# Kernel optimization log

Hardware: AMD Instinct MI355X
Metric: run time of the kernel (lower is better)

## Reference

```python
import jax, jax.numpy as jnp
import numpy as np
from jax import lax

T, Nn, K, IN, H1, H2, G, P, HEADS = 64, 2048, 32, 256, 128, 128, 256, 60, 3


def setup_inputs() -> dict:
    key = jax.random.key(0)
    ks = jax.random.split(key, 20)
    s = 0.05  # weight scale to keep activations sane
    return {
        'h': jax.random.normal(ks[0], (T, Nn, IN), jnp.float32),
        'neigh': jax.random.randint(ks[1], (Nn, K), 0, Nn),
        'Npop': jnp.ones((1,), jnp.float32) * 1e6,
        'I': jax.random.uniform(ks[2], (T,), jnp.float32) * 1e4,
        'R': jax.random.uniform(ks[3], (T,), jnp.float32) * 1e4,
        'S': jax.random.uniform(ks[4], (T,), jnp.float32) * 9e5,
        'It': jax.random.uniform(ks[5], (T,), jnp.float32),
        'Rt': jax.random.uniform(ks[6], (T,), jnp.float32),
        'fc1': jax.random.normal(ks[7], (HEADS, IN, H1), jnp.float32) * s,
        'fc2': jax.random.normal(ks[8], (HEADS * H1, H2), jnp.float32) * s,
        'gru_Wih': jax.random.normal(ks[9], (3 * G, H2), jnp.float32) * s,
        'gru_Whh': jax.random.normal(ks[10], (3 * G, G), jnp.float32) * s,
        'gru_bih': jax.random.normal(ks[11], (3 * G,), jnp.float32) * s,
        'gru_bhh': jax.random.normal(ks[12], (3 * G,), jnp.float32) * s,
        'res1_W': jax.random.normal(ks[13], (2 * P, G + 2), jnp.float32) * s,
        'res1_b': jax.random.normal(ks[14], (2 * P,), jnp.float32) * s,
        'res2_W': jax.random.normal(ks[15], (2, G + 2), jnp.float32) * s,
        'res2_b': jax.random.normal(ks[16], (2,), jnp.float32) * s,
        'hx0': jax.random.normal(ks[17], (G,), jnp.float32),
    }


def _input_attention(iz, neigh):
    # cosine^4 edge scores, unnormalized weighted sum of neighbor feats
    src = iz[neigh]                                  # [N,K,d]
    dot = jnp.einsum('nkd,nd->nk', src, iz)
    nsrc = jnp.sqrt(jnp.einsum('nkd,nkd->nk', src, src))
    ndst = jnp.sqrt(jnp.sum(iz * iz, axis=-1))[:, None]
    e = (dot / nsrc / ndst) ** 4                     # [N,K]
    return jnp.einsum('nk,nkd->nd', e, src)


def _gat_head(x, W, neigh):
    # dot-product edge attention + per-node softmax + weighted reduce
    z = x @ W                                        # [N,H]
    src = z[neigh]                                   # [N,K,H]
    e = jnp.einsum('nkd,nd->nk', src, z)             # [N,K]
    a = jax.nn.softmax(e, axis=1)
    return jnp.einsum('nk,nkd->nd', a, src)


def _gru_cell(x, hx, Wih, Whh, bih, bhh):
    gi = Wih @ x + bih                               # [3G]
    gh = Whh @ hx + bhh
    ir, iz, inn = jnp.split(gi, 3)
    hr, hz, hn = jnp.split(gh, 3)
    r = jax.nn.sigmoid(ir + hr)
    zg = jax.nn.sigmoid(iz + hz)
    n = jnp.tanh(inn + r * hn)
    return (1.0 - zg) * n + zg * hx


def reference(h, neigh, Npop, I, R, S, It, Rt, fc1, fc2, gru_Wih, gru_Whh,
              gru_bih, gru_bhh, res1_W, res1_b, res2_W, res2_b, hx0):
    Np = Npop[0]

    def step(hx, xs):
        h_t, I_t, R_t, S_t, It_t, Rt_t = xs
        ih = _input_attention(h_t, neigh)                       # [N,in]
        heads = jax.vmap(lambda W: _gat_head(ih, W, neigh))(fc1)  # [3,N,H1]
        c = jax.nn.relu(jnp.transpose(heads, (1, 0, 2)).reshape(Nn, HEADS * H1))
        c = _gat_head(c, fc2, neigh)                            # [N,H2]
        pooled = jnp.max(jax.nn.relu(c), axis=0)                # [H2]
        hx = _gru_cell(pooled, hx, gru_Wih, gru_Whh, gru_bih, gru_bhh)
        nhx = jnp.concatenate([hx, It_t[None], Rt_t[None]])     # [G+2]
        pred = res1_W @ nhx + res1_b                            # [2P]
        ab = res2_W @ nhx + res2_b
        a_s = jax.nn.sigmoid(ab[0])
        b_s = jax.nn.sigmoid(ab[1])
        new_I = pred[0::2]
        new_R = pred[1::2]

        def sir(st, _):
            lI, lR, lS = st
            dI = a_s * lI * (lS / Np) - b_s * lI
            dR = b_s * lI
            nI = lI + lax.stop_gradient(dI)
            nR = lR + lax.stop_gradient(dR)
            nS = Np - nI - nR
            return (nI, nR, nS), (dI, dR)

        _, (pI, pR) = lax.scan(sir, (I_t, R_t, S_t), None, length=P)
        return hx, (new_I, new_R, pI, pR)

    _, (new_I, new_R, phy_I, phy_R) = lax.scan(step, hx0, (h, I, R, S, It, Rt))
    return (new_I, new_R, phy_I.reshape(-1), phy_R.reshape(-1))
```

## Files before the change

### kernel.cpp

```cpp
#include <hip/hip_runtime.h>
#include <hip/hip_bf16.h>
#include <math.h>

#define T_STEPS 64
#define NN      2048
#define KN      32
#define IND     256
#define H1D     128
#define C1D     384
#define H2D     128
#define GD      256
#define PD      60
#define GRU_NB  8

#define BITREV5_INIT {0,16,8,24,4,20,12,28,2,18,10,26,6,22,14,30, \
                      1,17,9,25,5,21,13,29,3,19,11,27,7,23,15,31}

__device__ __forceinline__ float xpose_reduce16(float part[16], int lane) {
#pragma unroll
    for (int i = 0; i < 8; ++i) {
        float send = (lane & 2) ? part[i] : part[i + 8];
        float keep = (lane & 2) ? part[i + 8] : part[i];
        part[i] = keep + __shfl_xor(send, 2);
    }
#pragma unroll
    for (int i = 0; i < 4; ++i) {
        float send = (lane & 4) ? part[i] : part[i + 4];
        float keep = (lane & 4) ? part[i + 4] : part[i];
        part[i] = keep + __shfl_xor(send, 4);
    }
#pragma unroll
    for (int i = 0; i < 2; ++i) {
        float send = (lane & 8) ? part[i] : part[i + 2];
        float keep = (lane & 8) ? part[i + 2] : part[i];
        part[i] = keep + __shfl_xor(send, 8);
    }
    {
        float send = (lane & 16) ? part[0] : part[1];
        float keep = (lane & 16) ? part[1] : part[0];
        part[0] = keep + __shfl_xor(send, 16);
    }
    return part[0] + __shfl_xor(part[0], 32);
}

__global__ __launch_bounds__(256) void norms_kernel(const float* __restrict__ h,
                                                    float* __restrict__ norms,
                                                    int t_base) {
    int gw   = (int)((blockIdx.x * blockDim.x + threadIdx.x) >> 6);
    int lane = threadIdx.x & 63;
    int n    = gw & (NN - 1);
    int tloc = gw >> 11;
    const float* row = h + ((size_t)(t_base + tloc) * NN + n) * IND;
    float s = 0.f;
#pragma unroll
    for (int q = 0; q < 4; ++q) { float v = row[lane + 64 * q]; s += v * v; }
#pragma unroll
    for (int off = 32; off > 0; off >>= 1) s += __shfl_xor(s, off);
    if (lane == 0) norms[(size_t)tloc * NN + n] = sqrtf(s);
}

__global__ __launch_bounds__(256) void input_attn_kernel(const float* __restrict__ h,
                                                         const int* __restrict__ neigh,
                                                         const float* __restrict__ norms,
                                                         float* __restrict__ ih,
                                                         int t_base) {
    const int BR[32] = BITREV5_INIT;
    __shared__ float hd_s[2][2][32];
    int wave    = threadIdx.x >> 6;
    int nodeloc = wave >> 1;
    int half    = wave & 1;
    int lane    = threadIdx.x & 63;
    int gw   = (int)((blockIdx.x << 1) | nodeloc);
    int n    = gw & (NN - 1);
    int tloc = gw >> 11;
    const float* hT  = h + (size_t)(t_base + tloc) * NN * IND;
    const float* nrm = norms + (size_t)tloc * NN;

    const float* dst = hT + (size_t)n * IND + half * 128;
    float d0 = dst[lane], d1 = dst[lane + 64];

    int   jreg = neigh[n * KN + (lane & 31)];
    float nj   = nrm[jreg];
    float ndst = nrm[n];

    float r0[32], r1[32], comb[16];
#pragma unroll
    for (int i = 0; i < 16; ++i) {
        int ja = __shfl(jreg, BR[i]);
        int jb = __shfl(jreg, BR[i + 16]);
        const float* sa = hT + (size_t)ja * IND + half * 128;
        const float* sb = hT + (size_t)jb * IND + half * 128;
        r0[i]      = sa[lane]; r1[i]      = sa[lane + 64];
        r0[i + 16] = sb[lane]; r1[i + 16] = sb[lane + 64];
        float pa = r0[i] * d0 + r1[i] * d1;
        float pb = r0[i + 16] * d0 + r1[i + 16] * d1;
        float send = (lane & 1) ? pa : pb;
        float keep = (lane & 1) ? pb : pa;
        comb[i] = keep + __shfl_xor(send, 1);
    }
    float hdot = xpose_reduce16(comb, lane);
    if (lane < 32) hd_s[nodeloc][half][lane] = hdot;
    __syncthreads();
    float dot = hdot + hd_s[nodeloc][half ^ 1][lane & 31];

    float r  = dot / (nj * ndst);
    float r2 = r * r;
    float e  = r2 * r2;

    float a0 = 0.f, a1 = 0.f;
#pragma unroll
    for (int i = 0; i < 32; ++i) {
        float ek = __shfl(e, BR[i]);
        a0 += ek * r0[i];
        a1 += ek * r1[i];
    }
    float* orow = ih + (size_t)gw * IND + half * 128;
    orow[lane]      = a0;
    orow[lane + 64] = a1;
}

__global__ __launch_bounds__(256) void matmul_f32(const float* __restrict__ A,
                                                  const float* __restrict__ B,
                                                  float* __restrict__ C,
                                                  int M, int N, int K) {
    __shared__ float As[16][65];
    __shared__ float Bs[16][68];
    int tid  = threadIdx.x;
    int row0 = blockIdx.y * 64;
    int col0 = blockIdx.x * 64;
    int tr = tid >> 4, tc = tid & 15;
    float acc[4][4] = {};
    int la_m = tid >> 2;
    int la_k = (tid & 3) * 4;
    int lb_k = tid >> 4;
    int lb_n = (tid & 15) * 4;
    for (int k0 = 0; k0 < K; k0 += 16) {
        float4 av = *(const float4*)(A + (size_t)(row0 + la_m) * K + k0 + la_k);
        float4 bv = *(const float4*)(B + (size_t)(k0 + lb_k) * N + col0 + lb_n);
        __syncthreads();
        As[la_k + 0][la_m] = av.x; As[la_k + 1][la_m] = av.y;
        As[la_k + 2][la_m] = av.z; As[la_k + 3][la_m] = av.w;
        *(float4*)&Bs[lb_k][lb_n] = bv;
        __syncthreads();
#pragma unroll
        for (int kk = 0; kk < 16; ++kk) {
            float a[4], b[4];
#pragma unroll
            for (int r = 0; r < 4; ++r) a[r] = As[kk][tr * 4 + r];
#pragma unroll
            for (int c = 0; c < 4; ++c) b[c] = Bs[kk][tc * 4 + c];
#pragma unroll
            for (int r = 0; r < 4; ++r)
#pragma unroll
                for (int c = 0; c < 4; ++c) acc[r][c] += a[r] * b[c];
        }
    }
#pragma unroll
    for (int r = 0; r < 4; ++r) {
        float4 v = { acc[r][0], acc[r][1], acc[r][2], acc[r][3] };
        *(float4*)(C + (size_t)(row0 + tr * 4 + r) * N + col0 + tc * 4) = v;
    }
}

__global__ __launch_bounds__(192) void gat_heads_kernel(const float* __restrict__ z1,
                                                        const int* __restrict__ neigh,
                                                        float* __restrict__ c) {
    const int BR[32] = BITREV5_INIT;
    int n    = blockIdx.x & (NN - 1);
    const float* ztbl = z1 + (size_t)(blockIdx.x >> 11) * NN * C1D;
    int head = threadIdx.x >> 6;
    int lane = threadIdx.x & 63;

    const float* dst = ztbl + (size_t)n * C1D + head * H1D;
    float d0 = dst[lane], d1 = dst[lane + 64];
    int jreg = neigh[n * KN + (lane & 31)];

    float r0[32], r1[32], comb[16];
#pragma unroll
    for (int i = 0; i < 16; ++i) {
        int ja = __shfl(jreg, BR[i]);
        int jb = __shfl(jreg, BR[i + 16]);
        const float* sa = ztbl + (size_t)ja * C1D + head * H1D;
        const float* sb = ztbl + (size_t)jb * C1D + head * H1D;
        r0[i]      = sa[lane]; r1[i]      = sa[lane + 64];
        r0[i + 16] = sb[lane]; r1[i + 16] = sb[lane + 64];
        float pa = r0[i] * d0 + r1[i] * d1;
        float pb = r0[i + 16] * d0 + r1[i + 16] * d1;
        float send = (lane & 1) ? pa : pb;
        float keep = (lane & 1) ? pb : pa;
        comb[i] = keep + __shfl_xor(send, 1);
    }
    float dot = xpose_reduce16(comb, lane);

    float m = dot;
#pragma unroll
    for (int off = 16; off > 0; off >>= 1) m = fmaxf(m, __shfl_xor(m, off));
    float p = __expf(dot - m);
    float s = p;
#pragma unroll
    for (int off = 16; off > 0; off >>= 1) s += __shfl_xor(s, off);
    p /= s;

    float a0 = 0.f, a1 = 0.f;
#pragma unroll
    for (int i = 0; i < 32; ++i) {
        float pk = __shfl(p, BR[i]);
        a0 += pk * r0[i];
        a1 += pk * r1[i];
    }
    size_t base = (size_t)blockIdx.x * C1D + (size_t)head * H1D;
    c[base + lane]      = fmaxf(a0, 0.f);
    c[base + lane + 64] = fmaxf(a1, 0.f);
}

__global__ __launch_bounds__(256) void gat_final_kernel(const float* __restrict__ z2,
                                                        const int* __restrict__ neigh,
                                                        float* __restrict__ c2) {
    const int BR[32] = BITREV5_INIT;
    int gw   = (int)((blockIdx.x << 2) | (threadIdx.x >> 6));
    int n    = gw & (NN - 1);
    const float* ztbl = z2 + (size_t)(gw >> 11) * NN * H2D;
    int lane = threadIdx.x & 63;

    const float* dst = ztbl + (size_t)n * H2D;
    float d0 = dst[lane], d1 = dst[lane + 64];
    int jreg = neigh[n * KN + (lane & 31)];

    float r0[32], r1[32], comb[16];
#pragma unroll
    for (int i = 0; i < 16; ++i) {
        int ja = __shfl(jreg, BR[i]);
        int jb = __shfl(jreg, BR[i + 16]);
        const float* sa = ztbl + (size_t)ja * H2D;
        const float* sb = ztbl + (size_t)jb * H2D;
        r0[i]      = sa[lane]; r1[i]      = sa[lane + 64];
        r0[i + 16] = sb[lane]; r1[i + 16] = sb[lane + 64];
        float pa = r0[i] * d0 + r1[i] * d1;
        float pb = r0[i + 16] * d0 + r1[i + 16] * d1;
        float send = (lane & 1) ? pa : pb;
        float keep = (lane & 1) ? pb : pa;
        comb[i] = keep + __shfl_xor(send, 1);
    }
    float dot = xpose_reduce16(comb, lane);

    float m = dot;
#pragma unroll
    for (int off = 16; off > 0; off >>= 1) m = fmaxf(m, __shfl_xor(m, off));
    float p = __expf(dot - m);
    float s = p;
#pragma unroll
    for (int off = 16; off > 0; off >>= 1) s += __shfl_xor(s, off);
    p /= s;

    float a0 = 0.f, a1 = 0.f;
#pragma unroll
    for (int i = 0; i < 32; ++i) {
        float pk = __shfl(p, BR[i]);
        a0 += pk * r0[i];
        a1 += pk * r1[i];
    }
    c2[(size_t)gw * H2D + lane]      = fmaxf(a0, 0.f);
    c2[(size_t)gw * H2D + lane + 64] = fmaxf(a1, 0.f);
}

__global__ __launch_bounds__(128) void pool_part_kernel(const float* __restrict__ c2,
                                                        float* __restrict__ ppart) {
    int j = threadIdx.x;
    int tloc  = blockIdx.x >> 4;
    int slice = blockIdx.x & 15;
    const float* base = c2 + ((size_t)tloc * NN + slice * 128) * H2D;
    float mx = 0.f;
    for (int q = 0; q < 128; ++q) mx = fmaxf(mx, base[(size_t)q * H2D + j]);
    ppart[(size_t)blockIdx.x * H2D + j] = mx;
}
__global__ __launch_bounds__(128) void pool_reduce_kernel(const float* __restrict__ ppart,
                                                          float* __restrict__ pooled,
                                                          int t_base) {
    int j = threadIdx.x;
    const float* base = ppart + (size_t)blockIdx.x * 16 * H2D;
    float mx = 0.f;
#pragma unroll
    for (int q = 0; q < 16; ++q) mx = fmaxf(mx, base[(size_t)q * H2D + j]);
    pooled[(t_base + blockIdx.x) * H2D + j] = mx;
}

__global__ void prep_W1(const float* __restrict__ fc1, float* __restrict__ W1,
                        unsigned int* __restrict__ cnt) {
    int i = blockIdx.x * 256 + threadIdx.x;
    if (i < 256 * 384) {
        int d = i / 384, cf = i % 384;
        int hd = cf >> 7, j = cf & 127;
        W1[i] = fc1[(size_t)hd * 256 * 128 + (size_t)d * 128 + j];
    }
    if (i < T_STEPS) cnt[i] = 0u;
}

__global__ __launch_bounds__(256) void gi_all_kernel(const float* __restrict__ Wih,
                                                     const float* __restrict__ bih,
                                                     const float* __restrict__ pooled,
                                                     float* __restrict__ gi_all) {
    __shared__ float p_s[H2D];
    int t  = blockIdx.x / 3;
    int ob = (blockIdx.x % 3) * 256;
    if (threadIdx.x < H2D) p_s[threadIdx.x] = pooled[t * H2D + threadIdx.x];
    __syncthreads();
    int o = ob + threadIdx.x;
    float acc = bih[o];
    const float* wr = Wih + (size_t)o * H2D;
#pragma unroll 4
    for (int d = 0; d < H2D; ++d) acc += wr[d] * p_s[d];
    gi_all[t * 768 + o] = acc;
}

__global__ __launch_bounds__(768) void gru_reg_kernel(const float* __restrict__ Whh,
                                                      const float* __restrict__ bhh,
                                                      const float* __restrict__ gi_all,
                                                      const float* __restrict__ hx0,
                                                      float* hx_all,
                                                      unsigned int* cnt) {
    __shared__ float4 hx_pad[72];
    __shared__ __align__(16) float hx_lin[GD];
    __shared__ float gh_s[96];
    int b   = blockIdx.x;
    int tid = threadIdx.x;
    int row_local = tid >> 3;
    int sub       = tid & 7;
    int chunk     = row_local >> 5;
    int r_in      = row_local & 31;
    int grow      = chunk * GD + b * 32 + r_in;

    float4 wreg[8];
    const float4* wrow = (const float4*)(Whh + (size_t)grow * GD + sub * 32);
#pragma unroll
    for (int i = 0; i < 8; ++i) wreg[i] = wrow[i];
    float bias = (sub == 0) ? bhh[grow] : 0.f;

    for (int t = 0; t < T_STEPS; ++t) {
        if (t > 0) {
            if (tid == 0) {
                while (__hip_atomic_load(&cnt[t - 1], __ATOMIC_ACQUIRE,
                                         __HIP_MEMORY_SCOPE_AGENT) < GRU_NB)
                    __builtin_amdgcn_s_sleep(1);
            }
            __syncthreads();
        }
        const float* hsrc = (t == 0) ? hx0 : (hx_all + (size_t)(t - 1) * GD);
        if (tid < 64) {
            float4 v;
            v.x = __hip_atomic_load(hsrc + tid * 4 + 0, __ATOMIC_RELAXED, __HIP_MEMORY_SCOPE_AGENT);
            v.y = __hip_atomic_load(hsrc + tid * 4 + 1, __ATOMIC_RELAXED, __HIP_MEMORY_SCOPE_AGENT);
            v.z = __hip_atomic_load(hsrc + tid * 4 + 2, __ATOMIC_RELAXED, __HIP_MEMORY_SCOPE_AGENT);
            v.w = __hip_atomic_load(hsrc + tid * 4 + 3, __ATOMIC_RELAXED, __HIP_MEMORY_SCOPE_AGENT);
            hx_pad[(tid >> 3) * 9 + (tid & 7)] = v;
            ((float4*)hx_lin)[tid] = v;
        }
        __syncthreads();

        float acc = 0.f;
#pragma unroll
        for (int i = 0; i < 8; ++i) {
            float4 hv = hx_pad[sub * 9 + i];
            float4 wv = wreg[i];
            acc += wv.x * hv.x + wv.y * hv.y + wv.z * hv.z + wv.w * hv.w;
        }
        acc += __shfl_xor(acc, 1);
        acc += __shfl_xor(acc, 2);
        acc += __shfl_xor(acc, 4);
        if (sub == 0) gh_s[row_local] = acc + bias;
        __syncthreads();

        if (tid < 32) {
            int u = b * 32 + tid;
            float gi_r = gi_all[t * 768 + u];
            float gi_z = gi_all[t * 768 + 256 + u];
            float gi_n = gi_all[t * 768 + 512 + u];
            float r  = 1.f / (1.f + expf(-(gi_r + gh_s[tid])));
            float zg = 1.f / (1.f + expf(-(gi_z + gh_s[32 + tid])));
            float nn = tanhf(gi_n + r * gh_s[64 + tid]);
            float hnew = (1.f - zg) * nn + zg * hx_lin[u];
            __hip_atomic_store(&hx_all[(size_t)t * GD + u], hnew,
                               __ATOMIC_RELAXED, __HIP_MEMORY_SCOPE_AGENT);
            __threadfence();
        }
        __syncthreads();
        if (tid == 0)
            __hip_atomic_fetch_add(&cnt[t], 1u, __ATOMIC_RELEASE,
                                   __HIP_MEMORY_SCOPE_AGENT);
    }
}

__global__ __launch_bounds__(128) void res_sir_kernel(const float* __restrict__ hx_all,
                                                      const float* __restrict__ It,
                                                      const float* __restrict__ Rt,
                                                      const float* __restrict__ r1W,
                                                      const float* __restrict__ r1b,
                                                      const float* __restrict__ r2W,
                                                      const float* __restrict__ r2b,
                                                      const float* __restrict__ I,
                                                      const float* __restrict__ R,
                                                      const float* __restrict__ S,
                                                      const float* __restrict__ Npop,
                                                      float* __restrict__ out) {
    __shared__ float nhx[258];
    __shared__ float ab_s[2];
    int t = blockIdx.x, tid = threadIdx.x;
    for (int i = tid; i < GD; i += 128) nhx[i] = hx_all[t * GD + i];
    if (tid == 0) { nhx[256] = It[t]; nhx[257] = Rt[t]; }
    __syncthreads();
    if (tid < 120) {
        float acc = r1b[tid];
        const float* wr = r1W + tid * 258;
        for (int d = 0; d < 258; ++d) acc += wr[d] * nhx[d];
        int idx = t * 60 + (tid >> 1);
        if (tid & 1) out[3840 + idx] = acc;
        else         out[idx] = acc;
    }
    if (tid == 120 || tid == 121) {
        int q = tid - 120;
        float acc = r2b[q];
        const float* wr = r2W + q * 258;
        for (int d = 0; d < 258; ++d) acc += wr[d] * nhx[d];
        ab_s[q] = acc;
    }
    __syncthreads();
    if (tid == 0) {
        float a_s = 1.f / (1.f + expf(-ab_s[0]));
        float b_s = 1.f / (1.f + expf(-ab_s[1]));
        float Np = Npop[0];
        float lI = I[t], lR = R[t], lS = S[t];
        for (int p = 0; p < PD; ++p) {
            float dI = a_s * lI * (lS / Np) - b_s * lI;
            float dR = b_s * lI;
            lI += dI;
            lR += dR;
            lS = Np - lI - lR;
            out[7680  + t * 60 + p] = dI;
            out[11520 + t * 60 + p] = dR;
        }
    }
}

extern "C" void kernel_launch(void* const* d_in, const int* in_sizes, int n_in,
                              void* d_out, int out_size, void* d_ws, size_t ws_size,
                              hipStream_t stream) {
    const float* h    = (const float*)d_in[0];
    const int*   ng   = (const int*)  d_in[1];
    const float* Npop = (const float*)d_in[2];
    const float* I_   = (const float*)d_in[3];
    const float* R_   = (const float*)d_in[4];
    const float* S_   = (const float*)d_in[5];
    const float* It   = (const float*)d_in[6];
    const float* Rt   = (const float*)d_in[7];
    const float* fc1  = (const float*)d_in[8];
    const float* fc2  = (const float*)d_in[9];
    const float* gWih = (const float*)d_in[10];
    const float* gWhh = (const float*)d_in[11];
    const float* gbih = (const float*)d_in[12];
    const float* gbhh = (const float*)d_in[13];
    const float* r1W  = (const float*)d_in[14];
    const float* r1b  = (const float*)d_in[15];
    const float* r2W  = (const float*)d_in[16];
    const float* r2b  = (const float*)d_in[17];
    const float* hx0  = (const float*)d_in[18];
    float* out = (float*)d_out;

    char* w = (char*)d_ws;
    float* pooled = (float*)w; w += (size_t)T_STEPS * H2D * 4;
    float* hx_all = (float*)w; w += (size_t)T_STEPS * GD * 4;
    float* W1     = (float*)w; w += (size_t)256 * 384 * 4;
    float* gi_all = (float*)w; w += (size_t)T_STEPS * 768 * 4;
    float* ppart  = (float*)w; w += (size_t)T_STEPS * 16 * H2D * 4;
    unsigned int* cnt = (unsigned int*)w; w += 256;
    size_t fixed = (size_t)(w - (char*)d_ws);

    int Tc = 64;
    while (Tc > 1) {
        size_t need = fixed + (size_t)Tc * (8192 + 2ull * 2048 * 384 * 4);
        if (need <= ws_size) break;
        Tc >>= 1;
    }
    float* norms = (float*)w; w += (size_t)Tc * NN * 4;
    float* bufA  = (float*)w; w += (size_t)Tc * NN * C1D * 4;
    float* bufB  = (float*)w;

    prep_W1<<<(256 * 384 + 255) / 256, 256, 0, stream>>>(fc1, W1, cnt);

    for (int t0 = 0; t0 < T_STEPS; t0 += Tc) {
        int M = Tc * NN;
        norms_kernel      <<<Tc * NN / 4, 256, 0, stream>>>(h, norms, t0);
        input_attn_kernel <<<Tc * NN / 2, 256, 0, stream>>>(h, ng, norms, bufA, t0);
        matmul_f32<<<dim3(384 / 64, M / 64), 256, 0, stream>>>(bufA, W1, bufB, M, 384, 256);
        gat_heads_kernel  <<<Tc * NN, 192, 0, stream>>>(bufB, ng, bufA);
        matmul_f32<<<dim3(128 / 64, M / 64), 256, 0, stream>>>(bufA, fc2, bufB, M, 128, 384);
        gat_final_kernel  <<<Tc * NN / 4, 256, 0, stream>>>(bufB, ng, bufA);
        pool_part_kernel  <<<Tc * 16, 128, 0, stream>>>(bufA, ppart);
        pool_reduce_kernel<<<Tc, 128, 0, stream>>>(ppart, pooled, t0);
    }

    gi_all_kernel<<<T_STEPS * 3, 256, 0, stream>>>(gWih, gbih, pooled, gi_all);
    gru_reg_kernel<<<GRU_NB, 768, 0, stream>>>(gWhh, gbhh, gi_all, hx0, hx_all, cnt);
    res_sir_kernel<<<T_STEPS, 128, 0, stream>>>(hx_all, It, Rt, r1W, r1b, r2W, r2b,
                                                I_, R_, S_, Npop, out);
}
```

Baseline: 1.719 ms.

## Use readlane broadcasts, pin gathered rows in VGPRs, cap launch bounds, shrink chunk

The three gather-attention kernels now broadcast neighbor indices and attention weights with readlane (scalar) instead of ds_bpermute shuffles. An empty asm barrier keeps the gathered rows in VGPRs so the compiler cannot rematerialize the loads, and launch_bounds gains a min-blocks hint of 4. The time chunk Tc drops from 64 to 16, so the working buffers are smaller and may fit better in cache, at the cost of more kernel launches. The occupancy hint could force register spills given the 64+ live floats per thread.

```diff
diff --git a/kernel.cpp b/kernel.cpp
--- a/kernel.cpp
+++ b/kernel.cpp
@@ -16,6 +16,10 @@
 #define BITREV5_INIT {0,16,8,24,4,20,12,28,2,18,10,26,6,22,14,30, \
                       1,17,9,25,5,21,13,29,3,19,11,27,7,23,15,31}
 
+__device__ __forceinline__ float bcast_lane(float v, int lane_imm) {
+    return __uint_as_float(__builtin_amdgcn_readlane(__float_as_uint(v), lane_imm));
+}
+
 __device__ __forceinline__ float xpose_reduce16(float part[16], int lane) {
 #pragma unroll
     for (int i = 0; i < 8; ++i) {
@@ -59,11 +63,11 @@
     if (lane == 0) norms[(size_t)tloc * NN + n] = sqrtf(s);
 }
 
-__global__ __launch_bounds__(256) void input_attn_kernel(const float* __restrict__ h,
-                                                         const int* __restrict__ neigh,
-                                                         const float* __restrict__ norms,
-                                                         float* __restrict__ ih,
-                                                         int t_base) {
+__global__ __launch_bounds__(256, 4) void input_attn_kernel(const float* __restrict__ h,
+                                                            const int* __restrict__ neigh,
+                                                            const float* __restrict__ norms,
+                                                            float* __restrict__ ih,
+                                                            int t_base) {
     const int BR[32] = BITREV5_INIT;
     __shared__ float hd_s[2][2][32];
     int wave    = threadIdx.x >> 6;
@@ -86,10 +90,10 @@
     float r0[32], r1[32], comb[16];
 #pragma unroll
     for (int i = 0; i < 16; ++i) {
-        int ja = __shfl(jreg, BR[i]);
-        int jb = __shfl(jreg, BR[i + 16]);
-        const float* sa = hT + (size_t)ja * IND + half * 128;
-        const float* sb = hT + (size_t)jb * IND + half * 128;
+        int sja = __builtin_amdgcn_readlane(jreg, BR[i]);
+        int sjb = __builtin_amdgcn_readlane(jreg, BR[i + 16]);
+        const float* sa = hT + (size_t)sja * IND + half * 128;
+        const float* sb = hT + (size_t)sjb * IND + half * 128;
         r0[i]      = sa[lane]; r1[i]      = sa[lane + 64];
         r0[i + 16] = sb[lane]; r1[i + 16] = sb[lane + 64];
         float pa = r0[i] * d0 + r1[i] * d1;
@@ -98,6 +102,8 @@
         float keep = (lane & 1) ? pb : pa;
         comb[i] = keep + __shfl_xor(send, 1);
     }
+#pragma unroll
+    for (int i = 0; i < 32; ++i) asm volatile("" : "+v"(r0[i]), "+v"(r1[i]));
     float hdot = xpose_reduce16(comb, lane);
     if (lane < 32) hd_s[nodeloc][half][lane] = hdot;
     __syncthreads();
@@ -110,7 +116,7 @@
     float a0 = 0.f, a1 = 0.f;
 #pragma unroll
     for (int i = 0; i < 32; ++i) {
-        float ek = __shfl(e, BR[i]);
+        float ek = bcast_lane(e, BR[i]);
         a0 += ek * r0[i];
         a1 += ek * r1[i];
     }
@@ -162,9 +168,9 @@
     }
 }
 
-__global__ __launch_bounds__(192) void gat_heads_kernel(const float* __restrict__ z1,
-                                                        const int* __restrict__ neigh,
-                                                        float* __restrict__ c) {
+__global__ __launch_bounds__(192, 4) void gat_heads_kernel(const float* __restrict__ z1,
+                                                           const int* __restrict__ neigh,
+                                                           float* __restrict__ c) {
     const int BR[32] = BITREV5_INIT;
     int n    = blockIdx.x & (NN - 1);
     const float* ztbl = z1 + (size_t)(blockIdx.x >> 11) * NN * C1D;
@@ -178,10 +184,10 @@
     float r0[32], r1[32], comb[16];
 #pragma unroll
     for (int i = 0; i < 16; ++i) {
-        int ja = __shfl(jreg, BR[i]);
-        int jb = __shfl(jreg, BR[i + 16]);
-        const float* sa = ztbl + (size_t)ja * C1D + head * H1D;
-        const float* sb = ztbl + (size_t)jb * C1D + head * H1D;
+        int sja = __builtin_amdgcn_readlane(jreg, BR[i]);
+        int sjb = __builtin_amdgcn_readlane(jreg, BR[i + 16]);
+        const float* sa = ztbl + (size_t)sja * C1D + head * H1D;
+        const float* sb = ztbl + (size_t)sjb * C1D + head * H1D;
         r0[i]      = sa[lane]; r1[i]      = sa[lane + 64];
         r0[i + 16] = sb[lane]; r1[i + 16] = sb[lane + 64];
         float pa = r0[i] * d0 + r1[i] * d1;
@@ -190,6 +196,8 @@
         float keep = (lane & 1) ? pb : pa;
         comb[i] = keep + __shfl_xor(send, 1);
     }
+#pragma unroll
+    for (int i = 0; i < 32; ++i) asm volatile("" : "+v"(r0[i]), "+v"(r1[i]));
     float dot = xpose_reduce16(comb, lane);
 
     float m = dot;
@@ -204,7 +212,7 @@
     float a0 = 0.f, a1 = 0.f;
 #pragma unroll
     for (int i = 0; i < 32; ++i) {
-        float pk = __shfl(p, BR[i]);
+        float pk = bcast_lane(p, BR[i]);
         a0 += pk * r0[i];
         a1 += pk * r1[i];
     }
@@ -213,9 +221,9 @@
     c[base + lane + 64] = fmaxf(a1, 0.f);
 }
 
-__global__ __launch_bounds__(256) void gat_final_kernel(const float* __restrict__ z2,
-                                                        const int* __restrict__ neigh,
-                                                        float* __restrict__ c2) {
+__global__ __launch_bounds__(256, 4) void gat_final_kernel(const float* __restrict__ z2,
+                                                           const int* __restrict__ neigh,
+                                                           float* __restrict__ c2) {
     const int BR[32] = BITREV5_INIT;
     int gw   = (int)((blockIdx.x << 2) | (threadIdx.x >> 6));
     int n    = gw & (NN - 1);
@@ -229,10 +237,10 @@
     float r0[32], r1[32], comb[16];
 #pragma unroll
     for (int i = 0; i < 16; ++i) {
-        int ja = __shfl(jreg, BR[i]);
-        int jb = __shfl(jreg, BR[i + 16]);
-        const float* sa = ztbl + (size_t)ja * H2D;
-        const float* sb = ztbl + (size_t)jb * H2D;
+        int sja = __builtin_amdgcn_readlane(jreg, BR[i]);
+        int sjb = __builtin_amdgcn_readlane(jreg, BR[i + 16]);
+        const float* sa = ztbl + (size_t)sja * H2D;
+        const float* sb = ztbl + (size_t)sjb * H2D;
         r0[i]      = sa[lane]; r1[i]      = sa[lane + 64];
         r0[i + 16] = sb[lane]; r1[i + 16] = sb[lane + 64];
         float pa = r0[i] * d0 + r1[i] * d1;
@@ -241,6 +249,8 @@
         float keep = (lane & 1) ? pb : pa;
         comb[i] = keep + __shfl_xor(send, 1);
     }
+#pragma unroll
+    for (int i = 0; i < 32; ++i) asm volatile("" : "+v"(r0[i]), "+v"(r1[i]));
     float dot = xpose_reduce16(comb, lane);
 
     float m = dot;
@@ -255,7 +265,7 @@
     float a0 = 0.f, a1 = 0.f;
 #pragma unroll
     for (int i = 0; i < 32; ++i) {
-        float pk = __shfl(p, BR[i]);
+        float pk = bcast_lane(p, BR[i]);
         a0 += pk * r0[i];
         a1 += pk * r1[i];
     }
@@ -473,7 +483,7 @@
     unsigned int* cnt = (unsigned int*)w; w += 256;
     size_t fixed = (size_t)(w - (char*)d_ws);
 
-    int Tc = 64;
+    int Tc = 16;
     while (Tc > 1) {
         size_t need = fixed + (size_t)Tc * (8192 + 2ull * 2048 * 384 * 4);
         if (need <= ws_size) break;
```

Result: faster. 1.602 ms (-6.8%).
